# Performance work log

Hardware: AMD Instinct MI355X
Metric: run time of the kernel (lower is better)

Reference implementation:

```python
import jax, jax.numpy as jnp
import numpy as np

N = 20000   # nodes
E = 320000  # edges (before self loops)
IN = 128    # in_channel
H = 8       # heads
C = 128     # out_channels per head
HC = H * C  # 1024
G = 64      # graphs in batch


def _w(k, shape):
    s = 1.0 / np.sqrt(shape[-1])
    return jax.random.uniform(k, shape, jnp.float32, -s, s)


def setup_inputs() -> dict:
    key = jax.random.key(0)
    ks = jax.random.split(key, 12)
    return {
        "x": jax.random.normal(ks[0], (N, IN), jnp.float32),
        "edge_index": jax.random.randint(ks[1], (2, E), 0, N, dtype=jnp.int64),
        "batch": jnp.sort(jax.random.randint(ks[2], (N,), 0, G, dtype=jnp.int64)),
        # GATv2Conv params
        "Wl": _w(ks[3], (HC, IN)), "bl": jnp.zeros((HC,), jnp.float32),
        "Wr": _w(ks[4], (HC, IN)), "br": jnp.zeros((HC,), jnp.float32),
        "att": _w(ks[5], (H, C)),
        "Wres": _w(ks[6], (HC, IN)),
        "bias_conv": jnp.zeros((HC,), jnp.float32),
        # post-attention Linear(HC -> C)
        "Wlin": _w(ks[7], (C, HC)), "blin": jnp.zeros((C,), jnp.float32),
        # MLP head 128 -> 16 -> 32 -> 5
        "W1": _w(ks[8], (16, C)), "b1": jnp.zeros((16,), jnp.float32),
        "W2": _w(ks[9], (32, 16)), "b2": jnp.zeros((32,), jnp.float32),
        "W3": _w(ks[10], (5, 32)), "b3": jnp.zeros((5,), jnp.float32),
    }


def reference(x, edge_index, batch, Wl, bl, Wr, br, att, Wres, bias_conv,
              Wlin, blin, W1, b1, W2, b2, W3, b3):
    # --- GATv2Conv (PyG semantics: add_self_loops=True, concat=True, residual) ---
    loops = jnp.arange(N)
    src = jnp.concatenate([edge_index[0], loops])  # [E+N]
    dst = jnp.concatenate([edge_index[1], loops])
    x_l = (x @ Wl.T + bl).reshape(N, H, C)
    x_r = (x @ Wr.T + br).reshape(N, H, C)
    # per-edge attention logits
    e = jax.nn.leaky_relu(x_l[src] + x_r[dst], 0.2)        # [E+N, H, C]
    logits = jnp.einsum('ehc,hc->eh', e, att)              # [E+N, H]
    # segment softmax over destination neighborhoods
    m = jax.ops.segment_max(logits, dst, num_segments=N)
    a = jnp.exp(logits - m[dst])
    denom = jax.ops.segment_sum(a, dst, num_segments=N)
    alpha = a / (denom[dst] + 1e-16)                       # [E+N, H]
    # scatter-add weighted messages
    out = jax.ops.segment_sum(x_l[src] * alpha[:, :, None], dst,
                              num_segments=N).reshape(N, HC)
    out = out + x @ Wres.T + bias_conv                     # residual + bias
    # --- Linear + ELU ---
    h = jax.nn.elu(out @ Wlin.T + blin)                    # [N, C]
    # --- global mean pool per graph ---
    cnt = jax.ops.segment_sum(jnp.ones((N,), h.dtype), batch, num_segments=G)
    pooled = jax.ops.segment_sum(h, batch, num_segments=G) / jnp.maximum(cnt, 1.0)[:, None]
    # --- MLP head ---
    y = jax.nn.relu(pooled @ W1.T + b1)
    y = jax.nn.relu(y @ W2.T + b2)
    return y @ W3.T + b3                                   # [G, 5]
```

## Files before the change

kernel.cpp:

```cpp
#include <hip/hip_runtime.h>
#include <hip/hip_bf16.h>
#include <math.h>

#define N_NODES 20000
#define N_EDGES 320000
#define IN_CH   128
#define HEADS   8
#define CPH     128
#define HCH     1024
#define NG      64
#define ETOT    (N_EDGES + N_NODES)
#define NCVT    768
#define NROWT   157
#define GRID_P  (NROWT * 16)
#define PL      ((size_t)N_NODES * 128)

typedef __attribute__((ext_vector_type(8))) short s8v;
typedef __attribute__((ext_vector_type(4))) float f4v;
typedef __attribute__((ext_vector_type(8))) float f8v;
typedef __attribute__((ext_vector_type(4))) unsigned short u16x4;
typedef __attribute__((ext_vector_type(8))) unsigned short u16x8;

__device__ __forceinline__ unsigned short bf16_rne(float f) {
    unsigned u = __float_as_uint(f);
    unsigned r = u + 0x7fffu + ((u >> 16) & 1u);
    return (unsigned short)(r >> 16);
}
__device__ __forceinline__ float bf16_to_f(unsigned short h) {
    return __uint_as_float((unsigned)h << 16);
}

__global__ void init_kernel(int* __restrict__ deg, float* __restrict__ pooled) {
    int i = blockIdx.x * blockDim.x + threadIdx.x;
    if (i < N_NODES) deg[i] = 0;
    if (i < NG * CPH) pooled[i] = 0.0f;
}

__global__ void cvt_all(const float* __restrict__ x,  const float* __restrict__ Wl,
                        const float* __restrict__ Wr, const float* __restrict__ Wlin,
                        unsigned short* __restrict__ xhi,  unsigned short* __restrict__ xlo,
                        unsigned short* __restrict__ wlhi, unsigned short* __restrict__ wllo,
                        unsigned short* __restrict__ wrhi, unsigned short* __restrict__ wrlo,
                        unsigned short* __restrict__ wnhi, unsigned short* __restrict__ wnlo,
                        const int* __restrict__ ei, int* __restrict__ deg,
                        const float* __restrict__ Wres, const float* __restrict__ bias_conv,
                        const float* __restrict__ blin,
                        unsigned short* __restrict__ wchi, unsigned short* __restrict__ wclo,
                        float* __restrict__ bcomb)
{
    const int t = threadIdx.x;
    if (blockIdx.x < NCVT) {
        const int NX = N_NODES * IN_CH, NW = HCH * IN_CH;
        const int TOT4 = (NX + 3 * NW) >> 2;
        const int stride = NCVT * 256;
        for (int q = blockIdx.x * 256 + t; q < TOT4; q += stride) {
            int i = q << 2;
            const float* s; unsigned short *hi, *lo; int k;
            if (i < NX)               { s = x;    hi = xhi;  lo = xlo;  k = i; }
            else if (i < NX + NW)     { s = Wl;   hi = wlhi; lo = wllo; k = i - NX; }
            else if (i < NX + 2 * NW) { s = Wr;   hi = wrhi; lo = wrlo; k = i - NX - NW; }
            else                      { s = Wlin; hi = wnhi; lo = wnlo; k = i - NX - 2 * NW; }
            f4v f = *(const f4v*)&s[k];
            u16x4 h, l;
            #pragma unroll
            for (int e = 0; e < 4; ++e) {
                unsigned short hh = bf16_rne(f[e]);
                h[e] = hh;
                l[e] = bf16_rne(f[e] - bf16_to_f(hh));
            }
            *(u16x4*)&hi[k] = h;
            *(u16x4*)&lo[k] = l;
        }
        for (int e = blockIdx.x * 256 + t; e < ETOT; e += stride) {
            int dst = (e < N_EDGES) ? ei[N_EDGES + e] : (e - N_EDGES);
            atomicAdd(&deg[dst], 1);
        }
    } else if (t < 128) {
        const int j = blockIdx.x - NCVT;
        float s = 0.0f, pb = 0.0f;
        for (int m = 0; m < HCH; ++m) {
            float wl = Wlin[j * HCH + m];
            s  += wl * Wres[m * IN_CH + t];
            pb += wl * bias_conv[m];
        }
        unsigned short h = bf16_rne(s);
        wchi[j * IN_CH + t] = h;
        wclo[j * IN_CH + t] = bf16_rne(s - bf16_to_f(h));
        if (t == 0) bcomb[j] = blin[j] + pb;
    }
}

__global__ __launch_bounds__(256) void proj_gemm(
    const unsigned short* __restrict__ Ahi,
    const unsigned short* __restrict__ WLhi, const unsigned short* __restrict__ WLlo,
    const unsigned short* __restrict__ WRhi, const unsigned short* __restrict__ WRlo,
    const float* __restrict__ bl, const float* __restrict__ br,
    const float* __restrict__ att,
    unsigned short* __restrict__ xl_h, unsigned short* __restrict__ xr_h,
    float* __restrict__ dl, float* __restrict__ dr, int M)
{
    __shared__ unsigned short cst[128][136];
    const int id  = blockIdx.x;
    const int nat = (id & 7) * (GRID_P / 8) + (id >> 3);
    const int bx  = nat >> 4;
    const int by  = nat & 15;
    const int t    = threadIdx.x;
    const int wave = t >> 6, lane = t & 63;
    const int wr = wave >> 1, wc = wave & 1;
    const int l15 = lane & 15, lg = lane >> 4;
    const int m0 = bx * 128 + wr * 64;
    const int sel = by >> 3;
    const int hh  = by & 7;
    const int col0 = hh * 128;
    const unsigned short* Whi = sel ? WRhi : WLhi;
    const unsigned short* Wlo = sel ? WRlo : WLlo;
    const float* bias = sel ? br : bl;
    unsigned short* C = sel ? xr_h : xl_h;
    float* D = sel ? dr : dl;
    const int koff = lg * 8;
    const int K = IN_CH;

    int rowA[4], colB[4];
    #pragma unroll
    for (int i = 0; i < 4; ++i) { int r = m0 + i * 16 + l15; rowA[i] = r < M ? r : M - 1; }
    #pragma unroll
    for (int j = 0; j < 4; ++j) colB[j] = col0 + wc * 64 + j * 16 + l15;

    float bj[4];
    #pragma unroll
    for (int j = 0; j < 4; ++j) bj[j] = bias[colB[j]];

    f4v acc[4][4];
    #pragma unroll
    for (int i = 0; i < 4; ++i)
        #pragma unroll
        for (int j = 0; j < 4; ++j) acc[i][j] = (f4v){0.f, 0.f, 0.f, 0.f};

    for (int k0 = 0; k0 < K; k0 += 32) {
        s8v ah[4], bh[4], blv[4];
        #pragma unroll
        for (int i = 0; i < 4; ++i)
            ah[i] = *(const s8v*)&Ahi[(size_t)rowA[i] * K + k0 + koff];
        #pragma unroll
        for (int j = 0; j < 4; ++j) {
            size_t off = (size_t)colB[j] * K + k0 + koff;
            bh[j]  = *(const s8v*)&Whi[off];
            blv[j] = *(const s8v*)&Wlo[off];
        }
        #pragma unroll
        for (int i = 0; i < 4; ++i)
            #pragma unroll
            for (int j = 0; j < 4; ++j) {
                acc[i][j] = __builtin_amdgcn_mfma_f32_16x16x32_bf16(ah[i], bh[j],  acc[i][j], 0, 0, 0);
                acc[i][j] = __builtin_amdgcn_mfma_f32_16x16x32_bf16(ah[i], blv[j], acc[i][j], 0, 0, 0);
            }
    }

    #pragma unroll
    for (int i = 0; i < 4; ++i)
        #pragma unroll
        for (int r = 0; r < 4; ++r) {
            int lr = wr * 64 + i * 16 + lg * 4 + r;
            #pragma unroll
            for (int j = 0; j < 4; ++j)
                cst[lr][wc * 64 + j * 16 + l15] = bf16_rne(acc[i][j][r] + bj[j]);
        }
    __syncthreads();

    {
        const int c8  = (t & 15) * 8;
        const int r16 = t >> 4;
        #pragma unroll
        for (int it = 0; it < 8; ++it) {
            int lr = it * 16 + r16;
            int row = bx * 128 + lr;
            if (row >= M) continue;
            u16x8 v = *(const u16x8*)&cst[lr][c8];
            *(u16x8*)&C[(size_t)hh * PL + (size_t)row * 128 + c8] = v;
        }
    }

    {
        const int r2  = t >> 1;
        const int ch0 = (t & 1) * 64;
        float q = 0.0f;
        #pragma unroll
        for (int c = 0; c < 64; c += 8) {
            u16x8 cv = *(const u16x8*)&cst[r2][ch0 + c];
            f4v a0 = *(const f4v*)&att[hh * 128 + ch0 + c];
            f4v a1 = *(const f4v*)&att[hh * 128 + ch0 + c + 4];
            q = fmaf(a0[0], bf16_to_f(cv[0]), q);
            q = fmaf(a0[1], bf16_to_f(cv[1]), q);
            q = fmaf(a0[2], bf16_to_f(cv[2]), q);
            q = fmaf(a0[3], bf16_to_f(cv[3]), q);
            q = fmaf(a1[0], bf16_to_f(cv[4]), q);
            q = fmaf(a1[1], bf16_to_f(cv[5]), q);
            q = fmaf(a1[2], bf16_to_f(cv[6]), q);
            q = fmaf(a1[3], bf16_to_f(cv[7]), q);
        }
        q += __shfl_xor(q, 1, 64);
        int row = bx * 128 + r2;
        if ((t & 1) == 0 && row < M) D[hh * N_NODES + row] = q;
    }
}

__global__ __launch_bounds__(128) void mfma_gemm2(
    const unsigned short* __restrict__ A1h,
    const unsigned short* __restrict__ B1hi, const unsigned short* __restrict__ B1lo, int K1,
    const unsigned short* __restrict__ A2hi, const unsigned short* __restrict__ A2lo,
    const unsigned short* __restrict__ B2hi, const unsigned short* __restrict__ B2lo, int K2,
    const float* __restrict__ bias, const int* __restrict__ batch,
    float* __restrict__ pooled, int M)
{
    __shared__ float cst[32][130];
    __shared__ int batch_s[32];
    const int t    = threadIdx.x;
    const int wc   = t >> 6, lane = t & 63;
    const int l15 = lane & 15, lg = lane >> 4;
    const int m0 = blockIdx.x * 32;
    const int n0 = wc * 64;
    const int koff = lg * 8;

    if (t < 32) {
        int row = m0 + t;
        batch_s[t] = (row < M) ? batch[row] : -1;
    }

    int rowA[2], colB[4];
    #pragma unroll
    for (int i = 0; i < 2; ++i) { int r = m0 + i * 16 + l15; rowA[i] = r < M ? r : M - 1; }
    #pragma unroll
    for (int j = 0; j < 4; ++j) colB[j] = n0 + j * 16 + l15;

    float bj[4];
    #pragma unroll
    for (int j = 0; j < 4; ++j) bj[j] = bias[colB[j]];

    f4v acc[2][4];
    #pragma unroll
    for (int i = 0; i < 2; ++i)
        #pragma unroll
        for (int j = 0; j < 4; ++j) acc[i][j] = (f4v){0.f, 0.f, 0.f, 0.f};

    for (int k0 = 0; k0 < K1; k0 += 32) {
        s8v ah[2], bh[4], blv[4];
        #pragma unroll
        for (int i = 0; i < 2; ++i)
            ah[i] = *(const s8v*)&A1h[(size_t)rowA[i] * K1 + k0 + koff];
        #pragma unroll
        for (int j = 0; j < 4; ++j) {
            size_t off = (size_t)colB[j] * K1 + k0 + koff;
            bh[j]  = *(const s8v*)&B1hi[off];
            blv[j] = *(const s8v*)&B1lo[off];
        }
        #pragma unroll
        for (int i = 0; i < 2; ++i)
            #pragma unroll
            for (int j = 0; j < 4; ++j) {
                acc[i][j] = __builtin_amdgcn_mfma_f32_16x16x32_bf16(ah[i], bh[j],  acc[i][j], 0, 0, 0);
                acc[i][j] = __builtin_amdgcn_mfma_f32_16x16x32_bf16(ah[i], blv[j], acc[i][j], 0, 0, 0);
            }
    }
    for (int k0 = 0; k0 < K2; k0 += 32) {
        s8v ah[2], al[2], bh[4], blv[4];
        #pragma unroll
        for (int i = 0; i < 2; ++i) {
            size_t off = (size_t)rowA[i] * K2 + k0 + koff;
            ah[i] = *(const s8v*)&A2hi[off];
            al[i] = *(const s8v*)&A2lo[off];
        }
        #pragma unroll
        for (int j = 0; j < 4; ++j) {
            size_t off = (size_t)colB[j] * K2 + k0 + koff;
            bh[j]  = *(const s8v*)&B2hi[off];
            blv[j] = *(const s8v*)&B2lo[off];
        }
        #pragma unroll
        for (int i = 0; i < 2; ++i)
            #pragma unroll
            for (int j = 0; j < 4; ++j) {
                acc[i][j] = __builtin_amdgcn_mfma_f32_16x16x32_bf16(ah[i], bh[j],  acc[i][j], 0, 0, 0);
                acc[i][j] = __builtin_amdgcn_mfma_f32_16x16x32_bf16(ah[i], blv[j], acc[i][j], 0, 0, 0);
                acc[i][j] = __builtin_amdgcn_mfma_f32_16x16x32_bf16(al[i], bh[j],  acc[i][j], 0, 0, 0);
            }
    }

    #pragma unroll
    for (int i = 0; i < 2; ++i)
        #pragma unroll
        for (int r = 0; r < 4; ++r) {
            int lr = i * 16 + lg * 4 + r;
            #pragma unroll
            for (int j = 0; j < 4; ++j) {
                float v = acc[i][j][r] + bj[j];
                v = v > 0.0f ? v : expm1f(v);
                cst[lr][n0 + j * 16 + l15] = v;
            }
        }
    __syncthreads();

    const int col = t;
    if (col < 128) {
        float run = 0.0f;
        int cur_g = -2;
        #pragma unroll 4
        for (int r = 0; r < 32; ++r) {
            int g = batch_s[r];
            if (g != cur_g) {
                if (cur_g >= 0) atomicAdd(&pooled[cur_g * CPH + col], run);
                run = 0.0f; cur_g = g;
            }
            if (g >= 0) run += cst[r][col];
        }
        if (cur_g >= 0) atomicAdd(&pooled[cur_g * CPH + col], run);
    }
}

__global__ __launch_bounds__(256) void scan_kernel(
    const int* __restrict__ deg, int* __restrict__ rowptr, int* __restrict__ wof)
{
    __shared__ int wsum[4];
    __shared__ int carry_s;
    const int t = threadIdx.x, wave = t >> 6, lane = t & 63;
    if (t == 0) { carry_s = 0; rowptr[0] = 0; }
    __syncthreads();
    for (int base = 0; base < N_NODES; base += 1024) {
        int idx = base + t * 4;
        int d[4], p[4];
        #pragma unroll
        for (int k = 0; k < 4; ++k)
            d[k] = (idx + k < N_NODES) ? deg[idx + k] : 0;
        p[0] = d[0]; p[1] = p[0] + d[1]; p[2] = p[1] + d[2]; p[3] = p[2] + d[3];
        int v = p[3];
        #pragma unroll
        for (int off = 1; off < 64; off <<= 1) {
            int u = __shfl_up(v, off, 64);
            if (lane >= off) v += u;
        }
        if (lane == 63) wsum[wave] = v;
        __syncthreads();
        int woff = carry_s;
        #pragma unroll
        for (int w = 0; w < 4; ++w) if (w < wave) woff += wsum[w];
        int tbase = woff + v - p[3];
        #pragma unroll
        for (int k = 0; k < 4; ++k) {
            if (idx + k < N_NODES) {
                rowptr[idx + k + 1] = tbase + p[k];
                wof[idx + k] = tbase + p[k] - d[k];
            }
        }
        __syncthreads();
        if (t == 255) carry_s = woff + v;
        __syncthreads();
    }
}

__global__ void scatter_kernel(const int* __restrict__ ei, int* __restrict__ wof,
                               int* __restrict__ csr_src)
{
    for (int e = blockIdx.x * blockDim.x + threadIdx.x; e < ETOT;
         e += gridDim.x * blockDim.x) {
        int src, dst;
        if (e < N_EDGES) { src = ei[e]; dst = ei[N_EDGES + e]; }
        else             { src = dst = e - N_EDGES; }
        int p = atomicAdd(&wof[dst], 1);
        csr_src[p] = src;
    }
}

__global__ __launch_bounds__(256) void agg_fused(
    const unsigned short* __restrict__ xl_h, const unsigned short* __restrict__ xr_h,
    const float* __restrict__ att,
    const float* __restrict__ dl, const float* __restrict__ dr,
    const int* __restrict__ rowptr, const int* __restrict__ csr_src,
    unsigned short* __restrict__ agg_h)
{
    const int bid = blockIdx.x;
    const int h     = bid & 7;
    const int chunk = bid >> 3;
    const int t = threadIdx.x;
    const int dg = t >> 4;
    const int l  = t & 15;
    const int dst = chunk * 16 + dg;
    const size_t pbase = (size_t)h * PL + l * 8;
    const int beg = rowptr[dst], end = rowptr[dst + 1];

    const u16x8 bh8 = *(const u16x8*)&xr_h[pbase + (size_t)dst * 128];
    f8v b;
    #pragma unroll
    for (int e = 0; e < 8; ++e) b[e] = bf16_to_f(bh8[e]);
    f8v w04;
    {
        f4v a0 = *(const f4v*)&att[h * 128 + l * 8];
        f4v a1 = *(const f4v*)&att[h * 128 + l * 8 + 4];
        #pragma unroll
        for (int e = 0; e < 4; ++e) { w04[e] = 0.4f * a0[e]; w04[e + 4] = 0.4f * a1[e]; }
    }
    const float pb = 0.6f * dr[h * N_NODES + dst];

    float m = -__builtin_inff(), s = 0.0f;
    f8v acc = {0.f, 0.f, 0.f, 0.f, 0.f, 0.f, 0.f, 0.f};

    int j = beg;
    for (; j + 1 < end; j += 2) {
        const int s0 = csr_src[j], s1 = csr_src[j + 1];
        const u16x8 vh0 = *(const u16x8*)&xl_h[pbase + (size_t)s0 * 128];
        const u16x8 vh1 = *(const u16x8*)&xl_h[pbase + (size_t)s1 * 128];
        const float d0 = dl[h * N_NODES + s0], d1 = dl[h * N_NODES + s1];
        f8v v0, v1;
        #pragma unroll
        for (int e = 0; e < 8; ++e) { v0[e] = bf16_to_f(vh0[e]); v1[e] = bf16_to_f(vh1[e]); }

        float q0 = w04[0] * __builtin_fabsf(v0[0] + b[0]);
        float q1 = w04[0] * __builtin_fabsf(v1[0] + b[0]);
        #pragma unroll
        for (int e = 1; e < 8; ++e) {
            q0 = fmaf(w04[e], __builtin_fabsf(v0[e] + b[e]), q0);
            q1 = fmaf(w04[e], __builtin_fabsf(v1[e] + b[e]), q1);
        }
        #pragma unroll
        for (int off = 8; off; off >>= 1) {
            q0 += __shfl_xor(q0, off, 16);
            q1 += __shfl_xor(q1, off, 16);
        }
        const float p0 = fmaf(0.6f, d0, q0) + pb;
        const float p1 = fmaf(0.6f, d1, q1) + pb;

        const float mx = fmaxf(p0, p1);
        if (mx > m) {
            float scale = __expf(m - mx);
            float e0 = __expf(p0 - mx), e1 = __expf(p1 - mx);
            s = s * scale + e0 + e1;
            acc = acc * scale + v0 * e0 + v1 * e1;
            m = mx;
        } else {
            float e0 = __expf(p0 - m), e1 = __expf(p1 - m);
            s += e0 + e1;
            acc += v0 * e0 + v1 * e1;
        }
    }
    if (j < end) {
        const int s0 = csr_src[j];
        const u16x8 vh0 = *(const u16x8*)&xl_h[pbase + (size_t)s0 * 128];
        const float d0 = dl[h * N_NODES + s0];
        f8v v0;
        #pragma unroll
        for (int e = 0; e < 8; ++e) v0[e] = bf16_to_f(vh0[e]);
        float q0 = w04[0] * __builtin_fabsf(v0[0] + b[0]);
        #pragma unroll
        for (int e = 1; e < 8; ++e)
            q0 = fmaf(w04[e], __builtin_fabsf(v0[e] + b[e]), q0);
        #pragma unroll
        for (int off = 8; off; off >>= 1) q0 += __shfl_xor(q0, off, 16);
        const float p0 = fmaf(0.6f, d0, q0) + pb;
        if (p0 > m) {
            float scale = __expf(m - p0);
            s = s * scale + 1.0f;
            acc = acc * scale + v0;
            m = p0;
        } else {
            float e0 = __expf(p0 - m);
            s += e0;
            acc += v0 * e0;
        }
    }

    const float inv = 1.0f / (s + 1e-16f);
    f8v r = acc * inv;
    u16x8 hv;
    #pragma unroll
    for (int e = 0; e < 8; ++e) hv[e] = bf16_rne(r[e]);
    *(u16x8*)&agg_h[(size_t)dst * HCH + h * 128 + l * 8] = hv;
}

__global__ __launch_bounds__(128) void head_kernel(
    const float* __restrict__ pooled, const int* __restrict__ batch,
    const float* __restrict__ W1, const float* __restrict__ b1,
    const float* __restrict__ W2, const float* __restrict__ b2,
    const float* __restrict__ W3, const float* __restrict__ b3,
    float* __restrict__ out)
{
    __shared__ float sm_pool[128];
    __shared__ float sm_y1[16];
    __shared__ float sm_y2[32];
    const int g = blockIdx.x;
    const int t = threadIdx.x;

    int lo = 0, hi = N_NODES;
    while (lo < hi) { int mid = (lo + hi) >> 1; if (batch[mid] <  g) lo = mid + 1; else hi = mid; }
    const int s0 = lo;
    hi = N_NODES;
    while (lo < hi) { int mid = (lo + hi) >> 1; if (batch[mid] <= g) lo = mid + 1; else hi = mid; }
    const float inv = 1.0f / fmaxf((float)(lo - s0), 1.0f);

    sm_pool[t] = pooled[g * CPH + t] * inv;
    __syncthreads();

    {
        const int j  = t >> 3;
        const int c0 = (t & 7) * 16;
        float s = 0.0f;
        #pragma unroll
        for (int k = 0; k < 16; k += 4) {
            f4v wv = *(const f4v*)&W1[j * CPH + c0 + k];
            f4v pv = *(const f4v*)&sm_pool[c0 + k];
            s = fmaf(wv[0], pv[0], s); s = fmaf(wv[1], pv[1], s);
            s = fmaf(wv[2], pv[2], s); s = fmaf(wv[3], pv[3], s);
        }
        s += __shfl_xor(s, 1, 8);
        s += __shfl_xor(s, 2, 8);
        s += __shfl_xor(s, 4, 8);
        if ((t & 7) == 0) sm_y1[j] = fmaxf(s + b1[j], 0.0f);
    }
    __syncthreads();

    if (t < 32) {
        float s = b2[t];
        #pragma unroll
        for (int k = 0; k < 16; ++k) s = fmaf(W2[t * 16 + k], sm_y1[k], s);
        sm_y2[t] = fmaxf(s, 0.0f);
    }
    __syncthreads();

    if (t < 5) {
        float s = b3[t];
        #pragma unroll
        for (int k = 0; k < 32; ++k) s = fmaf(W3[t * 32 + k], sm_y2[k], s);
        out[g * 5 + t] = s;
    }
}

extern "C" void kernel_launch(void* const* d_in, const int* in_sizes, int n_in,
                              void* d_out, int out_size, void* d_ws, size_t ws_size,
                              hipStream_t stream)
{
    const float* x         = (const float*)d_in[0];
    const int*   ei        = (const int*)  d_in[1];
    const int*   batch     = (const int*)  d_in[2];
    const float* Wl        = (const float*)d_in[3];
    const float* bl        = (const float*)d_in[4];
    const float* Wr        = (const float*)d_in[5];
    const float* br        = (const float*)d_in[6];
    const float* att       = (const float*)d_in[7];
    const float* Wres      = (const float*)d_in[8];
    const float* bias_conv = (const float*)d_in[9];
    const float* Wlin      = (const float*)d_in[10];
    const float* blin      = (const float*)d_in[11];
    const float* W1        = (const float*)d_in[12];
    const float* b1        = (const float*)d_in[13];
    const float* W2        = (const float*)d_in[14];
    const float* b2        = (const float*)d_in[15];
    const float* W3        = (const float*)d_in[16];
    const float* b3        = (const float*)d_in[17];
    float* out = (float*)d_out;

    unsigned short* xl_h  = (unsigned short*)d_ws;
    unsigned short* xr_h  = xl_h + (size_t)N_NODES * HCH;
    unsigned short* agg_h = xr_h + (size_t)N_NODES * HCH;
    float* pooled = (float*)(agg_h + (size_t)N_NODES * HCH);
    float* bcomb  = pooled + NG * CPH;
    float* dl     = bcomb + 128;
    float* dr     = dl + (size_t)N_NODES * 8;
    unsigned short* x_hi  = (unsigned short*)(dr + (size_t)N_NODES * 8);
    unsigned short* x_lo  = x_hi  + (size_t)N_NODES * IN_CH;
    unsigned short* wl_hi = x_lo  + (size_t)N_NODES * IN_CH;
    unsigned short* wl_lo = wl_hi + HCH * IN_CH;
    unsigned short* wr_hi = wl_lo + HCH * IN_CH;
    unsigned short* wr_lo = wr_hi + HCH * IN_CH;
    unsigned short* wn_hi = wr_lo + HCH * IN_CH;
    unsigned short* wn_lo = wn_hi + CPH * HCH;
    unsigned short* wc_hi = wn_lo + CPH * HCH;
    unsigned short* wc_lo = wc_hi + CPH * IN_CH;
    int* deg     = (int*)(wc_lo + CPH * IN_CH);
    int* rowptr  = deg + N_NODES;
    int* wof     = rowptr + N_NODES + 1;
    int* csr_src = wof + N_NODES;

    init_kernel<<<(N_NODES + 255) / 256, 256, 0, stream>>>(deg, pooled);

    cvt_all<<<NCVT + 128, 256, 0, stream>>>(x, Wl, Wr, Wlin,
                                            x_hi, x_lo, wl_hi, wl_lo,
                                            wr_hi, wr_lo, wn_hi, wn_lo,
                                            ei, deg,
                                            Wres, bias_conv, blin,
                                            wc_hi, wc_lo, bcomb);

    proj_gemm<<<GRID_P, 256, 0, stream>>>(x_hi, wl_hi, wl_lo, wr_hi, wr_lo,
                                          bl, br, att, xl_h, xr_h, dl, dr, N_NODES);

    scan_kernel<<<1, 256, 0, stream>>>(deg, rowptr, wof);
    scatter_kernel<<<1024, 256, 0, stream>>>(ei, wof, csr_src);

    agg_fused<<<HEADS * (N_NODES / 16), 256, 0, stream>>>(xl_h, xr_h, att, dl, dr,
                                                          rowptr, csr_src, agg_h);

    dim3 g2((N_NODES + 31) / 32, 1);
    mfma_gemm2<<<g2, 128, 0, stream>>>(agg_h, wn_hi, wn_lo, HCH,
                                       x_hi, x_lo, wc_hi, wc_lo, IN_CH,
                                       bcomb, batch, pooled, N_NODES);

    head_kernel<<<NG, 128, 0, stream>>>(pooled, batch, W1, b1, W2, b2, W3, b3, out);
}
```

Baseline: 348.6 us.

## Split gemm2 K loop across two wave pairs and split aggregation launch

The second GEMM now runs 256 threads per block. One pair of waves handles the first half of the K=1024 range, and the other pair handles the second half plus the residual K=128 part. The partial sums are reduced through shared memory before bias, ELU and pooling. This is meant to raise the number of waves in flight and shorten the serial K loop, at the cost of extra LDS and one more barrier. The aggregation kernel is also split into two launches over node halves, which adds launch overhead and does not obviously help performance.

```diff
diff --git a/kernel.cpp b/kernel.cpp
--- a/kernel.cpp
+++ b/kernel.cpp
@@ -204,18 +204,21 @@
     }
 }
 
-__global__ __launch_bounds__(128) void mfma_gemm2(
+__global__ __launch_bounds__(256) void mfma_gemm2(
     const unsigned short* __restrict__ A1h,
-    const unsigned short* __restrict__ B1hi, const unsigned short* __restrict__ B1lo, int K1,
+    const unsigned short* __restrict__ B1hi, const unsigned short* __restrict__ B1lo,
     const unsigned short* __restrict__ A2hi, const unsigned short* __restrict__ A2lo,
-    const unsigned short* __restrict__ B2hi, const unsigned short* __restrict__ B2lo, int K2,
+    const unsigned short* __restrict__ B2hi, const unsigned short* __restrict__ B2lo,
     const float* __restrict__ bias, const int* __restrict__ batch,
     float* __restrict__ pooled, int M)
 {
     __shared__ float cst[32][130];
+    __shared__ float part[32][130];
     __shared__ int batch_s[32];
     const int t    = threadIdx.x;
-    const int wc   = t >> 6, lane = t & 63;
+    const int wave = t >> 6, lane = t & 63;
+    const int kw  = wave >> 1;
+    const int wc  = wave & 1;
     const int l15 = lane & 15, lg = lane >> 4;
     const int m0 = blockIdx.x * 32;
     const int n0 = wc * 64;
@@ -232,24 +235,22 @@
     #pragma unroll
     for (int j = 0; j < 4; ++j) colB[j] = n0 + j * 16 + l15;
 
-    float bj[4];
-    #pragma unroll
-    for (int j = 0; j < 4; ++j) bj[j] = bias[colB[j]];
-
     f4v acc[2][4];
     #pragma unroll
     for (int i = 0; i < 2; ++i)
         #pragma unroll
         for (int j = 0; j < 4; ++j) acc[i][j] = (f4v){0.f, 0.f, 0.f, 0.f};
 
-    for (int k0 = 0; k0 < K1; k0 += 32) {
+    const int k1beg = kw ? 512 : 0;
+    const int k1end = kw ? 1024 : 512;
+    for (int k0 = k1beg; k0 < k1end; k0 += 32) {
         s8v ah[2], bh[4], blv[4];
         #pragma unroll
         for (int i = 0; i < 2; ++i)
-            ah[i] = *(const s8v*)&A1h[(size_t)rowA[i] * K1 + k0 + koff];
+            ah[i] = *(const s8v*)&A1h[(size_t)rowA[i] * HCH + k0 + koff];
         #pragma unroll
         for (int j = 0; j < 4; ++j) {
-            size_t off = (size_t)colB[j] * K1 + k0 + koff;
+            size_t off = (size_t)colB[j] * HCH + k0 + koff;
             bh[j]  = *(const s8v*)&B1hi[off];
             blv[j] = *(const s8v*)&B1lo[off];
         }
@@ -261,46 +262,62 @@
                 acc[i][j] = __builtin_amdgcn_mfma_f32_16x16x32_bf16(ah[i], blv[j], acc[i][j], 0, 0, 0);
             }
     }
-    for (int k0 = 0; k0 < K2; k0 += 32) {
-        s8v ah[2], al[2], bh[4], blv[4];
-        #pragma unroll
-        for (int i = 0; i < 2; ++i) {
-            size_t off = (size_t)rowA[i] * K2 + k0 + koff;
-            ah[i] = *(const s8v*)&A2hi[off];
-            al[i] = *(const s8v*)&A2lo[off];
-        }
-        #pragma unroll
-        for (int j = 0; j < 4; ++j) {
-            size_t off = (size_t)colB[j] * K2 + k0 + koff;
-            bh[j]  = *(const s8v*)&B2hi[off];
-            blv[j] = *(const s8v*)&B2lo[off];
+    if (kw) {
+        for (int k0 = 0; k0 < IN_CH; k0 += 32) {
+            s8v ah[2], al[2], bh[4], blv[4];
+            #pragma unroll
+            for (int i = 0; i < 2; ++i) {
+                size_t off = (size_t)rowA[i] * IN_CH + k0 + koff;
+                ah[i] = *(const s8v*)&A2hi[off];
+                al[i] = *(const s8v*)&A2lo[off];
+            }
+            #pragma unroll
+            for (int j = 0; j < 4; ++j) {
+                size_t off = (size_t)colB[j] * IN_CH + k0 + koff;
+                bh[j]  = *(const s8v*)&B2hi[off];
+                blv[j] = *(const s8v*)&B2lo[off];
+            }
+            #pragma unroll
+            for (int i = 0; i < 2; ++i)
+                #pragma unroll
+                for (int j = 0; j < 4; ++j) {
+                    acc[i][j] = __builtin_amdgcn_mfma_f32_16x16x32_bf16(ah[i], bh[j],  acc[i][j], 0, 0, 0);
+                    acc[i][j] = __builtin_amdgcn_mfma_f32_16x16x32_bf16(ah[i], blv[j], acc[i][j], 0, 0, 0);
+                    acc[i][j] = __builtin_amdgcn_mfma_f32_16x16x32_bf16(al[i], bh[j],  acc[i][j], 0, 0, 0);
+                }
         }
         #pragma unroll
         for (int i = 0; i < 2; ++i)
             #pragma unroll
-            for (int j = 0; j < 4; ++j) {
-                acc[i][j] = __builtin_amdgcn_mfma_f32_16x16x32_bf16(ah[i], bh[j],  acc[i][j], 0, 0, 0);
-                acc[i][j] = __builtin_amdgcn_mfma_f32_16x16x32_bf16(ah[i], blv[j], acc[i][j], 0, 0, 0);
-                acc[i][j] = __builtin_amdgcn_mfma_f32_16x16x32_bf16(al[i], bh[j],  acc[i][j], 0, 0, 0);
-            }
-    }
-
-    #pragma unroll
-    for (int i = 0; i < 2; ++i)
-        #pragma unroll
-        for (int r = 0; r < 4; ++r) {
-            int lr = i * 16 + lg * 4 + r;
-            #pragma unroll
-            for (int j = 0; j < 4; ++j) {
-                float v = acc[i][j][r] + bj[j];
-                v = v > 0.0f ? v : expm1f(v);
-                cst[lr][n0 + j * 16 + l15] = v;
-            }
-        }
+            for (int r = 0; r < 4; ++r) {
+                int lr = i * 16 + lg * 4 + r;
+                #pragma unroll
+                for (int j = 0; j < 4; ++j)
+                    part[lr][n0 + j * 16 + l15] = acc[i][j][r];
+            }
+    }
     __syncthreads();
-
-    const int col = t;
-    if (col < 128) {
+    if (!kw) {
+        float bj[4];
+        #pragma unroll
+        for (int j = 0; j < 4; ++j) bj[j] = bias[colB[j]];
+        #pragma unroll
+        for (int i = 0; i < 2; ++i)
+            #pragma unroll
+            for (int r = 0; r < 4; ++r) {
+                int lr = i * 16 + lg * 4 + r;
+                #pragma unroll
+                for (int j = 0; j < 4; ++j) {
+                    float v = acc[i][j][r] + part[lr][n0 + j * 16 + l15] + bj[j];
+                    v = v > 0.0f ? v : expm1f(v);
+                    cst[lr][n0 + j * 16 + l15] = v;
+                }
+            }
+    }
+    __syncthreads();
+
+    if (t < 128) {
+        const int col = t;
         float run = 0.0f;
         int cur_g = -2;
         #pragma unroll 4
@@ -374,7 +391,7 @@
     const float* __restrict__ att,
     const float* __restrict__ dl, const float* __restrict__ dr,
     const int* __restrict__ rowptr, const int* __restrict__ csr_src,
-    unsigned short* __restrict__ agg_h)
+    unsigned short* __restrict__ agg_h, int dst0)
 {
     const int bid = blockIdx.x;
     const int h     = bid & 7;
@@ -382,7 +399,7 @@
     const int t = threadIdx.x;
     const int dg = t >> 4;
     const int l  = t & 15;
-    const int dst = chunk * 16 + dg;
+    const int dst = dst0 + chunk * 16 + dg;
     const size_t pbase = (size_t)h * PL + l * 8;
     const int beg = rowptr[dst], end = rowptr[dst + 1];
 
@@ -592,12 +609,14 @@
     scan_kernel<<<1, 256, 0, stream>>>(deg, rowptr, wof);
     scatter_kernel<<<1024, 256, 0, stream>>>(ei, wof, csr_src);
 
-    agg_fused<<<HEADS * (N_NODES / 16), 256, 0, stream>>>(xl_h, xr_h, att, dl, dr,
-                                                          rowptr, csr_src, agg_h);
+    agg_fused<<<HEADS * (N_NODES / 32), 256, 0, stream>>>(xl_h, xr_h, att, dl, dr,
+                                                          rowptr, csr_src, agg_h, 0);
+    agg_fused<<<HEADS * (N_NODES / 32), 256, 0, stream>>>(xl_h, xr_h, att, dl, dr,
+                                                          rowptr, csr_src, agg_h, N_NODES / 2);
 
     dim3 g2((N_NODES + 31) / 32, 1);
-    mfma_gemm2<<<g2, 128, 0, stream>>>(agg_h, wn_hi, wn_lo, HCH,
-                                       x_hi, x_lo, wc_hi, wc_lo, IN_CH,
+    mfma_gemm2<<<g2, 256, 0, stream>>>(agg_h, wn_hi, wn_lo,
+                                       x_hi, x_lo, wc_hi, wc_lo,
                                        bcomb, batch, pooled, N_NODES);
 
     head_kernel<<<NG, 128, 0, stream>>>(pooled, batch, W1, b1, W2, b2, W3, b3, out);
```

Measured after the change: 358.8 us. +2.9%, slower.
